# Performance work log

Hardware: AMD Instinct MI355X
Metric: run time of the kernel (lower is better)

Reference implementation:

```python
import math
import jax, jax.numpy as jnp
import numpy as np

K = 128  # num_kernels
H = 32   # num_heads
MAX_NODE_TYPE = 100
B = 4    # num graphs
N_PER_G = 512


def setup_inputs() -> dict:
    key = jax.random.key(0)
    ks = jax.random.split(key, 10)
    coord = jax.random.normal(ks[0], (B * N_PER_G, 3), dtype=jnp.float32)
    node_type = jax.random.randint(ks[1], (B * N_PER_G,), 0, MAX_NODE_TYPE + 1)
    gaussian_means = jax.random.uniform(ks[2], (1, K), minval=0.0, maxval=3.0, dtype=jnp.float32)
    gaussian_stds = jax.random.uniform(ks[3], (1, K), minval=0.0, maxval=3.0, dtype=jnp.float32)
    mul_w = jnp.zeros((MAX_NODE_TYPE + 1, 2), dtype=jnp.float32)   # init.constant_(mul, 0)
    bias_w = jnp.ones((MAX_NODE_TYPE + 1, 2), dtype=jnp.float32)   # init.constant_(bias, 1)
    W1 = jax.random.normal(ks[4], (K, K), dtype=jnp.float32) / math.sqrt(K)
    b1 = jax.random.normal(ks[5], (K,), dtype=jnp.float32) * 0.01
    W2 = jax.random.normal(ks[6], (H, K), dtype=jnp.float32) / math.sqrt(K)
    b2 = jax.random.normal(ks[7], (H,), dtype=jnp.float32) * 0.01
    return {
        "coord": coord, "node_type": node_type,
        "gaussian_means": gaussian_means, "gaussian_stds": gaussian_stds,
        "mul_w": mul_w, "bias_w": bias_w,
        "W1": W1, "b1": b1, "W2": W2, "b2": b2,
        "num_graphs": B, "num_nodes": N_PER_G,
    }


def _encode_graph(xg, ntg, mu, var, mul_w, bias_w, W1, b1, W2, b2):
    # xg: [n,3], ntg: [n]
    diff = xg[:, None, :] - xg[None, :, :]
    d2 = jnp.sum(diff * diff, axis=-1)                       # [n,n]
    dist = jnp.where(d2 > 0, jnp.sqrt(jnp.where(d2 > 0, d2, 1.0)), 0.0)
    me = mul_w[ntg]                                           # [n,2]
    be = bias_w[ntg]
    mul = me[:, 0][:, None] + me[None, :, 1]                  # [n,n]
    bias = be[:, 0][:, None] + be[None, :, 1]
    scaled = (mul * dist + bias)[..., None]                   # [n,n,K]
    gk = jnp.exp(-0.5 * jnp.square((scaled - mu) / var)) / (-math.sqrt(2.0 * math.pi) * var)
    h = jax.nn.gelu(gk @ W1.T + b1, approximate=False)        # exact GELU as in torch default
    return h @ W2.T + b2                                      # [n,n,H]


def reference(coord, node_type, gaussian_means, gaussian_stds, mul_w, bias_w,
              W1, b1, W2, b2, num_graphs, num_nodes):
    x = coord.reshape(num_graphs, num_nodes, 3)
    nt = node_type.reshape(num_graphs, num_nodes)
    mu = gaussian_means.reshape(-1)                           # [K]
    var = jnp.abs(gaussian_stds.reshape(-1)) + 0.01           # [K]
    enc = lambda xg, ntg: _encode_graph(xg, ntg, mu, var, mul_w, bias_w, W1, b1, W2, b2)
    return jax.vmap(enc)(x, nt)                               # [B,n,n,H]
```

## Files before the change

kernel.cpp:

```cpp
#include <hip/hip_runtime.h>

#define NGRAPH 4
#define NNODE  512
#define NTOT   2048
#define KK     128
#define HH     32
#define TAB_T  4096
#define NPAIR  (NGRAPH*NNODE*NNODE)
#define MMB    1024

#define BLK_OFF  16
#define NODE_OFF (BLK_OFF + 2*MMB)
#define W1T_OFF  (NODE_OFF + NTOT*8)
#define W2T_OFF  (W1T_OFF + KK*KK)
#define B1_OFF   (W2T_OFF + KK*HH)
#define B2_OFF   (B1_OFF + KK)
#define MU_OFF   (B2_OFF + HH)
#define VAR_OFF  (MU_OFF + KK)
#define TAB_OFF  39424

__device__ __forceinline__ float bf2f(unsigned short h) {
    return __uint_as_float(((unsigned)h) << 16);
}
__device__ __forceinline__ unsigned short f2bf(float f) {
    unsigned u = __float_as_uint(f);
    u += 0x7FFFu + ((u >> 16) & 1u);
    return (unsigned short)(u >> 16);
}
__device__ __forceinline__ unsigned pk2(float a, float b) {
    return (unsigned)f2bf(a) | ((unsigned)f2bf(b) << 16);
}
__device__ __forceinline__ float ldf(const void* p, int i, bool bf) {
    return bf ? bf2f(((const unsigned short*)p)[i]) : ((const float*)p)[i];
}
__device__ __forceinline__ float gelu_exact(float x) {
    return x * 0.5f * (1.0f + erff(x * 0.7071067811865476f));
}
__device__ __forceinline__ float pair_s(const float* __restrict__ ws, int g, int i, int j) {
    const float4* ri = (const float4*)(ws + NODE_OFF + (size_t)(g*NNODE + i)*8);
    const float4* rj = (const float4*)(ws + NODE_OFF + (size_t)(g*NNODE + j)*8);
    const float4 ai = ri[0], bi = ri[1];
    const float4 aj = rj[0], bj = rj[1];
    const float dx = ai.x - aj.x, dy = ai.y - aj.y, dz = ai.z - aj.z;
    const float d2 = dx*dx + dy*dy + dz*dz;
    const float dist = (d2 > 0.0f) ? sqrtf(d2) : 0.0f;
    return (ai.w + bj.x) * dist + (bi.y + bj.z);
}

__global__ void k_prep(const void* coord, const int* __restrict__ ntype,
                       const void* means, const void* stds,
                       const void* mulw, const void* biasw,
                       const void* W1, const void* b1,
                       const void* W2, const void* b2,
                       float* __restrict__ ws) {
    const bool bf = (((const unsigned*)biasw)[0] == 0x3F803F80u);
    const int t = blockIdx.x * blockDim.x + threadIdx.x;
    if (t < NTOT) {
        const int nt = ntype[t];
        float* rec = ws + NODE_OFF + t * 8;
        rec[0] = ldf(coord, t*3+0, bf);
        rec[1] = ldf(coord, t*3+1, bf);
        rec[2] = ldf(coord, t*3+2, bf);
        rec[3] = ldf(mulw,  nt*2+0, bf);
        rec[4] = ldf(mulw,  nt*2+1, bf);
        rec[5] = ldf(biasw, nt*2+0, bf);
        rec[6] = ldf(biasw, nt*2+1, bf);
        rec[7] = 0.0f;
    } else if (t < NTOT + KK*KK) {
        const int m = t - NTOT;
        const int k = m >> 7, j = m & (KK-1);
        ws[W1T_OFF + m] = ldf(W1, j*KK + k, bf);
    } else if (t < NTOT + KK*KK + KK*HH) {
        const int m = t - NTOT - KK*KK;
        const int j = m >> 5, ch = m & (HH-1);
        ws[W2T_OFF + m] = ldf(W2, ch*KK + j, bf);
    } else if (t < NTOT + KK*KK + KK*HH + KK) {
        const int m = t - NTOT - KK*KK - KK*HH;
        ws[B1_OFF + m] = ldf(b1, m, bf);
    } else if (t < NTOT + KK*KK + KK*HH + KK + HH) {
        const int m = t - NTOT - KK*KK - KK*HH - KK;
        ws[B2_OFF + m] = ldf(b2, m, bf);
    } else if (t < NTOT + KK*KK + KK*HH + KK + HH + KK) {
        const int m = t - NTOT - KK*KK - KK*HH - KK - HH;
        ws[MU_OFF + m] = ldf(means, m, bf);
    } else if (t < NTOT + KK*KK + KK*HH + KK + HH + 2*KK) {
        const int m = t - NTOT - KK*KK - KK*HH - KK - HH - KK;
        ws[VAR_OFF + m] = fabsf(ldf(stds, m, bf)) + 0.01f;
    }
}

__global__ __launch_bounds__(256) void k_minmax(float* __restrict__ ws) {
    __shared__ float smn[4], smx[4];
    float mn = 1e30f, mx = -1e30f;
    for (int p = blockIdx.x * 256 + threadIdx.x; p < NPAIR; p += MMB * 256) {
        const int j = p & (NNODE-1);
        const int i = (p >> 9) & (NNODE-1);
        const int g = p >> 18;
        const float s = pair_s(ws, g, i, j);
        mn = fminf(mn, s); mx = fmaxf(mx, s);
    }
    #pragma unroll
    for (int off = 32; off > 0; off >>= 1) {
        mn = fminf(mn, __shfl_xor(mn, off, 64));
        mx = fmaxf(mx, __shfl_xor(mx, off, 64));
    }
    const int wv = threadIdx.x >> 6;
    if ((threadIdx.x & 63) == 0) { smn[wv] = mn; smx[wv] = mx; }
    __syncthreads();
    if (threadIdx.x == 0) {
        mn = fminf(fminf(smn[0], smn[1]), fminf(smn[2], smn[3]));
        mx = fmaxf(fmaxf(smx[0], smx[1]), fmaxf(smx[2], smx[3]));
        ws[BLK_OFF + 2*blockIdx.x]     = mn;
        ws[BLK_OFF + 2*blockIdx.x + 1] = mx;
    }
}

__global__ __launch_bounds__(256) void k_reduce2(float* __restrict__ ws) {
    __shared__ float smn[4], smx[4];
    float mn = 1e30f, mx = -1e30f;
    for (int b = threadIdx.x; b < MMB; b += 256) {
        mn = fminf(mn, ws[BLK_OFF + 2*b]);
        mx = fmaxf(mx, ws[BLK_OFF + 2*b + 1]);
    }
    #pragma unroll
    for (int off = 32; off > 0; off >>= 1) {
        mn = fminf(mn, __shfl_xor(mn, off, 64));
        mx = fmaxf(mx, __shfl_xor(mx, off, 64));
    }
    const int wv = threadIdx.x >> 6;
    if ((threadIdx.x & 63) == 0) { smn[wv] = mn; smx[wv] = mx; }
    __syncthreads();
    if (threadIdx.x == 0) {
        ws[0] = fminf(fminf(smn[0], smn[1]), fminf(smn[2], smn[3]));
        ws[1] = fmaxf(fmaxf(smx[0], smx[1]), fmaxf(smx[2], smx[3]));
    }
}

__global__ __launch_bounds__(128) void k_table(float* __restrict__ ws) {
    __shared__ float g_s[KK][4];
    __shared__ float h_s[4][KK];
    const int tid = threadIdx.x;
    const float lo = ws[0], hi = ws[1];
    float width = hi - lo;
    if (!(width > 1e-6f)) width = 1e-6f;
    const float step = width * (1.0f / (float)(TAB_T - 1));
    const int e0 = blockIdx.x * 4;

    {
        const float mu  = ws[MU_OFF + tid];
        const float var = ws[VAR_OFF + tid];
        const float inv = 1.0f / var;
        const float amp = -0.3989422804014327f * inv;
        #pragma unroll
        for (int e = 0; e < 4; ++e) {
            const float s = lo + (float)(e0 + e) * step;
            const float z = (s - mu) * inv;
            g_s[tid][e] = amp * expf(-0.5f * z * z);
        }
    }
    __syncthreads();
    float a0 = ws[B1_OFF + tid], a1 = a0, a2 = a0, a3 = a0;
    for (int k = 0; k < KK; ++k) {
        const float w = ws[W1T_OFF + k*KK + tid];
        const float4 gv = *(const float4*)g_s[k];
        a0 += w * gv.x; a1 += w * gv.y; a2 += w * gv.z; a3 += w * gv.w;
    }
    h_s[0][tid] = gelu_exact(a0);
    h_s[1][tid] = gelu_exact(a1);
    h_s[2][tid] = gelu_exact(a2);
    h_s[3][tid] = gelu_exact(a3);
    __syncthreads();
    const int e = tid >> 5, ch = tid & (HH-1);
    float acc = ws[B2_OFF + ch];
    for (int j = 0; j < KK; ++j)
        acc += ws[W2T_OFF + j*HH + ch] * h_s[e][j];
    ws[TAB_OFF + (size_t)(e0 + e)*HH + ch] = acc;
}

__global__ __launch_bounds__(256) void k_apply(const float* __restrict__ ws,
                                               const void* __restrict__ biasw,
                                               void* __restrict__ out) {
    const bool bf = (((const unsigned*)biasw)[0] == 0x3F803F80u);
    const int p = blockIdx.x * blockDim.x + threadIdx.x;
    const int j = p & (NNODE-1);
    const int i = (p >> 9) & (NNODE-1);
    const int g = p >> 18;
    const float s = pair_s(ws, g, i, j);

    const float lo = ws[0], hi = ws[1];
    float width = hi - lo;
    if (!(width > 1e-6f)) width = 1e-6f;
    float u = (s - lo) * ((float)(TAB_T - 1) / width);
    u = fminf(fmaxf(u, 0.0f), (float)(TAB_T - 1));
    int i0 = (int)u;
    if (i0 > TAB_T - 2) i0 = TAB_T - 2;
    const float f = u - (float)i0;

    const float4* t0 = (const float4*)(ws + TAB_OFF + (size_t)i0 * HH);
    if (bf) {
        uint4* op = (uint4*)((unsigned short*)out + (size_t)p * HH);
        #pragma unroll
        for (int q = 0; q < 4; ++q) {
            const float4 a0 = t0[2*q],     b0 = t0[2*q + 8];
            const float4 a1 = t0[2*q + 1], b1 = t0[2*q + 9];
            uint4 w;
            w.x = pk2(a0.x + f*(b0.x - a0.x), a0.y + f*(b0.y - a0.y));
            w.y = pk2(a0.z + f*(b0.z - a0.z), a0.w + f*(b0.w - a0.w));
            w.z = pk2(a1.x + f*(b1.x - a1.x), a1.y + f*(b1.y - a1.y));
            w.w = pk2(a1.z + f*(b1.z - a1.z), a1.w + f*(b1.w - a1.w));
            op[q] = w;
        }
    } else {
        float4* op = (float4*)((float*)out + (size_t)p * HH);
        #pragma unroll
        for (int q = 0; q < 8; ++q) {
            const float4 a = t0[q], b = t0[q + 8];
            op[q] = make_float4(a.x + f*(b.x - a.x), a.y + f*(b.y - a.y),
                                a.z + f*(b.z - a.z), a.w + f*(b.w - a.w));
        }
    }
}

extern "C" void kernel_launch(void* const* d_in, const int* in_sizes, int n_in,
                              void* d_out, int out_size, void* d_ws, size_t ws_size,
                              hipStream_t stream) {
    const void* coord = d_in[0];
    const int*  ntype = (const int*)d_in[1];
    const void* means = d_in[2];
    const void* stds  = d_in[3];
    const void* mulw  = d_in[4];
    const void* biasw = d_in[5];
    const void* W1    = d_in[6];
    const void* b1    = d_in[7];
    const void* W2    = d_in[8];
    const void* b2    = d_in[9];
    float* ws = (float*)d_ws;

    k_prep<<<90, 256, 0, stream>>>(coord, ntype, means, stds, mulw, biasw, W1, b1, W2, b2, ws);
    k_minmax<<<MMB, 256, 0, stream>>>(ws);
    k_reduce2<<<1, 256, 0, stream>>>(ws);
    k_table<<<TAB_T/4, 128, 0, stream>>>(ws);
    k_apply<<<NPAIR/256, 256, 0, stream>>>(ws, biasw, d_out);
}
```

Baseline: 203.3 us.

## Fold final min/max reduction into table kernel and split pair output across four threads

The single-block reduce kernel is removed: every table block now reduces the per-block min/max partials itself, and block 0 writes the global range for the apply kernel. The apply kernel uses four threads per pair, each interpolating and writing one quarter of the 32 output channels, so stores are more coalesced and more threads are in flight. The cost is that each pair's distance and table index are recomputed four times, and the partial reduction is repeated in every table block.

```diff
diff --git a/kernel.cpp b/kernel.cpp
--- a/kernel.cpp
+++ b/kernel.cpp
@@ -115,10 +115,14 @@
     }
 }
 
-__global__ __launch_bounds__(256) void k_reduce2(float* __restrict__ ws) {
-    __shared__ float smn[4], smx[4];
+__global__ __launch_bounds__(128) void k_table(float* __restrict__ ws) {
+    __shared__ float g_s[KK][4];
+    __shared__ float h_s[4][KK];
+    __shared__ float wmn[2], wmx[2];
+    const int tid = threadIdx.x;
+
     float mn = 1e30f, mx = -1e30f;
-    for (int b = threadIdx.x; b < MMB; b += 256) {
+    for (int b = tid; b < MMB; b += 128) {
         mn = fminf(mn, ws[BLK_OFF + 2*b]);
         mx = fmaxf(mx, ws[BLK_OFF + 2*b + 1]);
     }
@@ -127,20 +131,12 @@
         mn = fminf(mn, __shfl_xor(mn, off, 64));
         mx = fmaxf(mx, __shfl_xor(mx, off, 64));
     }
-    const int wv = threadIdx.x >> 6;
-    if ((threadIdx.x & 63) == 0) { smn[wv] = mn; smx[wv] = mx; }
-    __syncthreads();
-    if (threadIdx.x == 0) {
-        ws[0] = fminf(fminf(smn[0], smn[1]), fminf(smn[2], smn[3]));
-        ws[1] = fmaxf(fmaxf(smx[0], smx[1]), fmaxf(smx[2], smx[3]));
-    }
-}
-
-__global__ __launch_bounds__(128) void k_table(float* __restrict__ ws) {
-    __shared__ float g_s[KK][4];
-    __shared__ float h_s[4][KK];
-    const int tid = threadIdx.x;
-    const float lo = ws[0], hi = ws[1];
+    if ((tid & 63) == 0) { wmn[tid >> 6] = mn; wmx[tid >> 6] = mx; }
+    __syncthreads();
+    const float lo = fminf(wmn[0], wmn[1]);
+    const float hi = fmaxf(wmx[0], wmx[1]);
+    if (blockIdx.x == 0 && tid == 0) { ws[0] = lo; ws[1] = hi; }
+
     float width = hi - lo;
     if (!(width > 1e-6f)) width = 1e-6f;
     const float step = width * (1.0f / (float)(TAB_T - 1));
@@ -181,7 +177,9 @@
                                                const void* __restrict__ biasw,
                                                void* __restrict__ out) {
     const bool bf = (((const unsigned*)biasw)[0] == 0x3F803F80u);
-    const int p = blockIdx.x * blockDim.x + threadIdx.x;
+    const int gid = blockIdx.x * blockDim.x + threadIdx.x;
+    const int q = gid & 3;
+    const int p = gid >> 2;
     const int j = p & (NNODE-1);
     const int i = (p >> 9) & (NNODE-1);
     const int g = p >> 18;
@@ -197,27 +195,21 @@
     const float f = u - (float)i0;
 
     const float4* t0 = (const float4*)(ws + TAB_OFF + (size_t)i0 * HH);
+    const float4 a0 = t0[2*q],     c0 = t0[2*q + 8];
+    const float4 a1 = t0[2*q + 1], c1 = t0[2*q + 9];
+    const float r0 = a0.x + f*(c0.x - a0.x), r1 = a0.y + f*(c0.y - a0.y);
+    const float r2 = a0.z + f*(c0.z - a0.z), r3 = a0.w + f*(c0.w - a0.w);
+    const float r4 = a1.x + f*(c1.x - a1.x), r5 = a1.y + f*(c1.y - a1.y);
+    const float r6 = a1.z + f*(c1.z - a1.z), r7 = a1.w + f*(c1.w - a1.w);
     if (bf) {
-        uint4* op = (uint4*)((unsigned short*)out + (size_t)p * HH);
-        #pragma unroll
-        for (int q = 0; q < 4; ++q) {
-            const float4 a0 = t0[2*q],     b0 = t0[2*q + 8];
-            const float4 a1 = t0[2*q + 1], b1 = t0[2*q + 9];
-            uint4 w;
-            w.x = pk2(a0.x + f*(b0.x - a0.x), a0.y + f*(b0.y - a0.y));
-            w.y = pk2(a0.z + f*(b0.z - a0.z), a0.w + f*(b0.w - a0.w));
-            w.z = pk2(a1.x + f*(b1.x - a1.x), a1.y + f*(b1.y - a1.y));
-            w.w = pk2(a1.z + f*(b1.z - a1.z), a1.w + f*(b1.w - a1.w));
-            op[q] = w;
-        }
+        uint4 w;
+        w.x = pk2(r0, r1); w.y = pk2(r2, r3);
+        w.z = pk2(r4, r5); w.w = pk2(r6, r7);
+        ((uint4*)((unsigned short*)out + (size_t)p * HH))[q] = w;
     } else {
-        float4* op = (float4*)((float*)out + (size_t)p * HH);
-        #pragma unroll
-        for (int q = 0; q < 8; ++q) {
-            const float4 a = t0[q], b = t0[q + 8];
-            op[q] = make_float4(a.x + f*(b.x - a.x), a.y + f*(b.y - a.y),
-                                a.z + f*(b.z - a.z), a.w + f*(b.w - a.w));
-        }
+        float4* op = (float4*)((float*)out + (size_t)p * HH) + 2*q;
+        op[0] = make_float4(r0, r1, r2, r3);
+        op[1] = make_float4(r4, r5, r6, r7);
     }
 }
 
@@ -238,7 +230,6 @@
 
     k_prep<<<90, 256, 0, stream>>>(coord, ntype, means, stds, mulw, biasw, W1, b1, W2, b2, ws);
     k_minmax<<<MMB, 256, 0, stream>>>(ws);
-    k_reduce2<<<1, 256, 0, stream>>>(ws);
     k_table<<<TAB_T/4, 128, 0, stream>>>(ws);
-    k_apply<<<NPAIR/256, 256, 0, stream>>>(ws, biasw, d_out);
-}
+    k_apply<<<(NPAIR*4)/256, 256, 0, stream>>>(ws, biasw, d_out);
+}
```

After: 183.3 us. -9.8%, faster.
